# Performance work log

Measured on AMD Instinct MI355X. Metric: run time of the kernel, lower is better.

Reference implementation:

```python
import math
import jax, jax.numpy as jnp
import numpy as np

FACTOR = 5
N_HEADS = 8


def setup_inputs() -> dict:
    key = jax.random.key(0)
    ks = jax.random.split(key, 9)
    B, S, D = 4, 8192, 512
    s = 0.02
    x = jax.random.normal(ks[0], (B, S, D), jnp.float32)
    Wq = jax.random.normal(ks[1], (D, D), jnp.float32) * s
    bq = jax.random.normal(ks[2], (D,), jnp.float32) * s
    Wk = jax.random.normal(ks[3], (D, D), jnp.float32) * s
    bk = jax.random.normal(ks[4], (D,), jnp.float32) * s
    Wv = jax.random.normal(ks[5], (D, D), jnp.float32) * s
    bv = jax.random.normal(ks[6], (D,), jnp.float32) * s
    Wo = jax.random.normal(ks[7], (D, D), jnp.float32) * s
    bo = jax.random.normal(ks[8], (D,), jnp.float32) * s
    return {"x": x, "Wq": Wq, "bq": bq, "Wk": Wk, "bk": bk,
            "Wv": Wv, "bv": bv, "Wo": Wo, "bo": bo}


def reference(x, Wq, bq, Wk, bk, Wv, bv, Wo, bo):
    B, S, D = x.shape
    H = N_HEADS
    hd = D // H
    scale = hd ** -0.5

    def proj(W, b):
        # [B,S,D] -> [B,H,S,hd]
        return (x @ W + b).reshape(B, S, H, hd).transpose(0, 2, 1, 3)

    q = proj(Wq, bq)
    k = proj(Wk, bk)
    v = proj(Wv, bv)

    # number of "active" queries: O(log S)
    sampled = max(1, min(S, int(FACTOR * math.log(S + 1))))

    sparsity = jnp.sum(q * q, axis=-1)                    # [B,H,S]
    top_idx = jax.lax.top_k(sparsity, sampled)[1]         # [B,H,u]

    sel_q = jnp.take_along_axis(q, top_idx[..., None], axis=2)  # [B,H,u,hd]
    scores = jnp.einsum('bhud,bhsd->bhus', sel_q, k) * scale     # [B,H,u,S]
    attn = jax.nn.softmax(scores, axis=-1)
    sel_ctx = jnp.einsum('bhus,bhsd->bhud', attn, v)             # [B,H,u,hd]

    # default context = mean of values; overwrite rows of selected queries
    ctx = jnp.broadcast_to(v.mean(axis=2, keepdims=True), (B, H, S, hd))
    bi = jnp.arange(B)[:, None, None]
    hi = jnp.arange(H)[None, :, None]
    ctx = ctx.at[bi, hi, top_idx].set(sel_ctx)                   # scatter [B,H,S,hd]

    ctx = ctx.transpose(0, 2, 1, 3).reshape(B, S, D)
    return ctx @ Wo + bo
```

## Files before the change

### kernel.cpp

```cpp
#include <hip/hip_runtime.h>
#include <hip/hip_fp16.h>
#include <math.h>

#define B_ 4
#define S_ 8192
#define D_ 512
#define H_ 8
#define U_ 45
#define NCHUNK 16

typedef unsigned short ushortT;
typedef __attribute__((ext_vector_type(8))) _Float16 half8;
typedef __attribute__((ext_vector_type(4))) float f32x4;

__device__ __forceinline__ ushortT f2h(float f) {
    return __half_as_ushort(__float2half(f));
}
__device__ __forceinline__ float h2f(ushortT u) {
    return __half2float(__ushort_as_half(u));
}

__device__ __forceinline__ void gload_lds16(const ushortT* g, ushortT* l) {
    __builtin_amdgcn_global_load_lds(
        (const __attribute__((address_space(1))) void*)g,
        (__attribute__((address_space(3))) void*)l,
        16, 0, 0);
}

__global__ __launch_bounds__(256) void xconv(
    const float* __restrict__ X, ushortT* __restrict__ Xf,
    float* __restrict__ vsum, float* __restrict__ outbase)
{
    if (blockIdx.x == 0) {
        float4 z = {0.f, 0.f, 0.f, 0.f};
        *(float4*)&vsum[threadIdx.x * 8]        = z;
        *(float4*)&vsum[threadIdx.x * 8 + 4]    = z;
        *(float4*)&outbase[threadIdx.x * 8]     = z;
        *(float4*)&outbase[threadIdx.x * 8 + 4] = z;
    }
    size_t i = ((size_t)blockIdx.x * 256 + threadIdx.x) * 8;
    float4 a = *(const float4*)(X + i);
    float4 b = *(const float4*)(X + i + 4);
    *(ushort4*)(Xf + i)     = make_ushort4(f2h(a.x), f2h(a.y), f2h(a.z), f2h(a.w));
    *(ushort4*)(Xf + i + 4) = make_ushort4(f2h(b.x), f2h(b.y), f2h(b.z), f2h(b.w));
}

__global__ __launch_bounds__(256) void wprep(
    const float* __restrict__ Wq, const float* __restrict__ Wk,
    const float* __restrict__ Wv,
    ushortT* __restrict__ WqT, ushortT* __restrict__ WkT,
    ushortT* __restrict__ WvT)
{
    __shared__ float t[32][33];
    const int z = blockIdx.z;
    const float* W = (z == 0) ? Wq : (z == 1) ? Wk : Wv;
    ushortT* O = (z == 0) ? WqT : (z == 1) ? WkT : WvT;
    const int tx = threadIdx.x & 31, ty4 = (threadIdx.x >> 5) * 4;
    const int r0 = blockIdx.y * 32, c0 = blockIdx.x * 32;
#pragma unroll
    for (int i = 0; i < 4; ++i)
        t[ty4 + i][tx] = W[(size_t)(r0 + ty4 + i) * 512 + c0 + tx];
    __syncthreads();
#pragma unroll
    for (int i = 0; i < 4; ++i)
        O[(size_t)(c0 + ty4 + i) * 512 + r0 + tx] = f2h(t[tx][ty4 + i]);
}

__global__ __launch_bounds__(256, 2) void qkv_mfma(
    const ushortT* __restrict__ Xf,
    const ushortT* __restrict__ WqT, const ushortT* __restrict__ WkT,
    const ushortT* __restrict__ WvT,
    const float* __restrict__ bq, const float* __restrict__ bk,
    const float* __restrict__ bv,
    ushortT* __restrict__ Qbuf, ushortT* __restrict__ Kbuf,
    ushortT* __restrict__ VT,
    float* __restrict__ sparsity, float* __restrict__ vsum)
{
    __shared__ ushortT lds[2 * 128 * 64];
    ushortT* As = lds;
    ushortT* Bs = lds + 8192;

    const int tid  = threadIdx.x;
    const int w    = tid >> 6, lane = tid & 63;
    const int quad = lane >> 4, c16 = lane & 15;
    const int wr   = w >> 1,  wc  = w & 1;
    const int mat  = blockIdx.y >> 2;
    const int nt   = blockIdx.y & 3;
    const int m0   = blockIdx.x * 128;
    const int n0   = nt * 128;

    const int srowL = lane >> 3;
    const int slc   = (((lane & 7) - (srowL & 7)) & 7) * 8;
    const int rrot  = c16 & 7;

    const ushortT* Ag = (mat == 2) ? WvT : Xf;
    const ushortT* Bg = (mat == 0) ? WqT : (mat == 1) ? WkT : Xf;
    const int arow0 = (mat == 2) ? n0 : m0;
    const int brow0 = (mat == 2) ? m0 : n0;

    f32x4 acc[4][4];
#pragma unroll
    for (int i = 0; i < 4; ++i)
#pragma unroll
        for (int j = 0; j < 4; ++j) acc[i][j] = (f32x4){0.f, 0.f, 0.f, 0.f};

    for (int k0 = 0; k0 < 512; k0 += 64) {
        __syncthreads();
#pragma unroll
        for (int c = 0; c < 4; ++c) {
            const int R = c * 32 + w * 8 + srowL;
            const int lbase = c * 2048 + w * 512;
            gload_lds16(Ag + (size_t)(arow0 + R) * 512 + k0 + slc, As + lbase);
            gload_lds16(Bg + (size_t)(brow0 + R) * 512 + k0 + slc, Bs + lbase);
        }
        __syncthreads();
#pragma unroll
        for (int kk = 0; kk < 2; ++kk) {
            const int phk = (((kk * 4 + quad) + rrot) & 7) * 8;
            half8 af[4], bf[4];
#pragma unroll
            for (int i = 0; i < 4; ++i) {
                af[i] = *(const half8*)&As[(wr * 64 + i * 16 + c16) * 64 + phk];
                bf[i] = *(const half8*)&Bs[(wc * 64 + i * 16 + c16) * 64 + phk];
            }
#pragma unroll
            for (int i = 0; i < 4; ++i)
#pragma unroll
                for (int j = 0; j < 4; ++j)
                    acc[i][j] = __builtin_amdgcn_mfma_f32_16x16x32_f16(af[i], bf[j], acc[i][j], 0, 0, 0);
        }
    }

    if (mat == 0) {
        const int b = m0 >> 13;
        const int head = (n0 + wc * 64) >> 6;
        float bb[4];
#pragma unroll
        for (int j = 0; j < 4; ++j) bb[j] = bq[n0 + wc * 64 + j * 16 + c16];
        ushortT* qbase = Qbuf + ((size_t)(b * 8 + head) * 8192) * 64;
#pragma unroll
        for (int i = 0; i < 4; ++i)
#pragma unroll
            for (int r = 0; r < 4; ++r) {
                const int s = (m0 & 8191) + wr * 64 + i * 16 + quad * 4 + r;
                float p = 0.f;
#pragma unroll
                for (int j = 0; j < 4; ++j) {
                    float v = acc[i][j][r] + bb[j];
                    qbase[(size_t)s * 64 + j * 16 + c16] = f2h(v);
                    p = fmaf(v, v, p);
                }
                p += __shfl_xor(p, 1);
                p += __shfl_xor(p, 2);
                p += __shfl_xor(p, 4);
                p += __shfl_xor(p, 8);
                if (c16 == 0)
                    sparsity[((size_t)b * H_ + head) * S_ + s] = p;
            }
    } else if (mat == 1) {
        const int b = m0 >> 13;
        const int head = (n0 + wc * 64) >> 6;
        float bb[4];
#pragma unroll
        for (int j = 0; j < 4; ++j) bb[j] = bk[n0 + wc * 64 + j * 16 + c16];
        ushortT* kbase = Kbuf + ((size_t)(b * 8 + head) * 8192) * 64;
#pragma unroll
        for (int i = 0; i < 4; ++i)
#pragma unroll
            for (int r = 0; r < 4; ++r) {
                const int s = (m0 & 8191) + wr * 64 + i * 16 + quad * 4 + r;
#pragma unroll
                for (int j = 0; j < 4; ++j)
                    kbase[(size_t)s * 64 + j * 16 + c16] = f2h(acc[i][j][r] + bb[j]);
            }
    } else {
        const int b = m0 >> 13;
        const int sbase = (m0 & 8191) + wc * 64;
#pragma unroll
        for (int i = 0; i < 4; ++i)
#pragma unroll
            for (int r = 0; r < 4; ++r) {
                const int dcol = n0 + wr * 64 + i * 16 + quad * 4 + r;
                const int head = dcol >> 6, dd = dcol & 63;
                const float biasv = bv[dcol];
                ushortT* vrow = VT + ((size_t)(b * 8 + head) * 64 + dd) * 8192;
                float vsa = 0.f;
#pragma unroll
                for (int j = 0; j < 4; ++j) {
                    float v = acc[i][j][r] + biasv;
                    vrow[sbase + j * 16 + c16] = f2h(v);
                    vsa += v;
                }
                vsa += __shfl_xor(vsa, 1);
                vsa += __shfl_xor(vsa, 2);
                vsa += __shfl_xor(vsa, 4);
                vsa += __shfl_xor(vsa, 8);
                if (c16 == 0) atomicAdd(&vsum[b * 512 + dcol], vsa);
            }
    }
}

__global__ __launch_bounds__(256) void topk_kernel(
    const float* __restrict__ sparsity, int* __restrict__ topidx)
{
    __shared__ unsigned vals[S_];
    __shared__ unsigned hist[8][256];
    __shared__ int ssum[256];
    __shared__ unsigned prefix_s;
    __shared__ int need_s;
    __shared__ int cnt_gt_s, cnt_eq_s;
    __shared__ int eqidx[64];
    const int bh = blockIdx.x, tid = threadIdx.x;
    const unsigned* sp = (const unsigned*)(sparsity + (size_t)bh * S_);
    for (int i = tid; i < S_; i += 256) vals[i] = sp[i];

    unsigned prefix = 0;
    int need = U_;
    const int rep = tid & 7;
    for (int level = 0; level < 4; ++level) {
        const int shift = 24 - level * 8;
#pragma unroll
        for (int r = 0; r < 8; ++r) hist[r][tid] = 0;
        __syncthreads();
        const unsigned pmask = (level == 0) ? 0u : (0xFFFFFFFFu << (shift + 8));
        for (int i = tid; i < S_; i += 256) {
            unsigned v = vals[i];
            if ((v & pmask) == prefix)
                atomicAdd(&hist[rep][(v >> shift) & 255], 1u);
        }
        __syncthreads();
        int bs = 0;
#pragma unroll
        for (int r = 0; r < 8; ++r) bs += (int)hist[r][tid];
        ssum[tid] = bs;
        __syncthreads();
        for (int off = 1; off < 256; off <<= 1) {
            int add = (tid + off < 256) ? ssum[tid + off] : 0;
            __syncthreads();
            ssum[tid] += add;
            __syncthreads();
        }
        int snext = (tid == 255) ? 0 : ssum[tid + 1];
        if (ssum[tid] >= need && snext < need) {
            prefix_s = prefix | ((unsigned)tid << shift);
            need_s = need - snext;
        }
        __syncthreads();
        prefix = prefix_s;
        need = need_s;
        __syncthreads();
    }
    const unsigned T = prefix;
    if (tid == 0) { cnt_gt_s = 0; cnt_eq_s = 0; }
    __syncthreads();
    for (int i = tid; i < S_; i += 256) {
        unsigned v = vals[i];
        if (v > T) {
            int p = atomicAdd(&cnt_gt_s, 1);
            topidx[bh * U_ + p] = i;
        } else if (v == T) {
            int p = atomicAdd(&cnt_eq_s, 1);
            if (p < 64) eqidx[p] = i;
        }
    }
    __syncthreads();
    if (tid == 0) {
        int rem = U_ - cnt_gt_s;
        int n = cnt_eq_s < 64 ? cnt_eq_s : 64;
        for (int a = 0; a < rem; ++a) {
            int best = 1 << 30, bj = 0;
            for (int j = 0; j < n; ++j)
                if (eqidx[j] < best) { best = eqidx[j]; bj = j; }
            topidx[bh * U_ + cnt_gt_s + a] = best;
            eqidx[bj] = 1 << 30;
        }
    }
}

__global__ __launch_bounds__(256, 2) void attn_mfma(
    const ushortT* __restrict__ Qbuf, const ushortT* __restrict__ Kbuf,
    const ushortT* __restrict__ VT, const int* __restrict__ topidx,
    float* __restrict__ pl, float* __restrict__ pacc)
{
    __shared__ float sc[48 * 132];
    __shared__ ushortT Qb[48 * 72];

    const int tid = threadIdx.x;
    const int w = tid >> 6, lane = tid & 63;
    const int quad = lane >> 4, c16 = lane & 15;
    const int bh = blockIdx.y;
    const int s_base = blockIdx.x * 512;

    for (int i = tid; i < 48 * 64; i += 256) {
        int q = i >> 6, d = i & 63;
        float v = 0.f;
        if (q < U_) {
            int s = topidx[bh * U_ + q];
            v = h2f(Qbuf[((size_t)bh * 8192 + s) * 64 + d]) * 0.125f;
        }
        Qb[q * 72 + d] = f2h(v);
    }

    f32x4 O[3];
#pragma unroll
    for (int mt = 0; mt < 3; ++mt) O[mt] = (f32x4){0.f, 0.f, 0.f, 0.f};
    float lacc[12];
#pragma unroll
    for (int qi = 0; qi < 12; ++qi) lacc[qi] = 0.f;

    __syncthreads();

    half8 qa[3][2];
#pragma unroll
    for (int mt = 0; mt < 3; ++mt)
#pragma unroll
        for (int kk = 0; kk < 2; ++kk)
            qa[mt][kk] = *(const half8*)&Qb[(mt * 16 + c16) * 72 + kk * 32 + quad * 8];

    const ushortT* kb  = Kbuf + (size_t)bh * 8192 * 64;
    const ushortT* vtb = VT + ((size_t)bh * 64 + w * 16 + c16) * 8192;

    for (int ci = 0; ci < 4; ++ci) {
        const int s0 = s_base + ci * 128;

        half8 kf[2][2];
#pragma unroll
        for (int nt2 = 0; nt2 < 2; ++nt2)
#pragma unroll
            for (int kk = 0; kk < 2; ++kk)
                kf[nt2][kk] = *(const half8*)&kb[
                    (size_t)(s0 + w * 32 + nt2 * 16 + c16) * 64 + kk * 32 + quad * 8];
        f32x4 sacc[3][2];
#pragma unroll
        for (int mt = 0; mt < 3; ++mt)
#pragma unroll
            for (int nt2 = 0; nt2 < 2; ++nt2) {
                sacc[mt][nt2] = (f32x4){0.f, 0.f, 0.f, 0.f};
#pragma unroll
                for (int kk = 0; kk < 2; ++kk)
                    sacc[mt][nt2] = __builtin_amdgcn_mfma_f32_16x16x32_f16(
                        qa[mt][kk], kf[nt2][kk], sacc[mt][nt2], 0, 0, 0);
            }
#pragma unroll
        for (int mt = 0; mt < 3; ++mt)
#pragma unroll
            for (int nt2 = 0; nt2 < 2; ++nt2)
#pragma unroll
                for (int r = 0; r < 4; ++r)
                    sc[(mt * 16 + quad * 4 + r) * 132 + w * 32 + nt2 * 16 + c16] =
                        sacc[mt][nt2][r];
        __syncthreads();

        half8 vb[4];
#pragma unroll
        for (int kk = 0; kk < 4; ++kk)
            vb[kk] = *(const half8*)&vtb[s0 + kk * 32 + quad * 8];

#pragma unroll
        for (int qi = 0; qi < 12; ++qi) {
            const int q = w * 12 + qi;
            float x0 = sc[q * 132 + lane];
            float x1 = sc[q * 132 + 64 + lane];
            ushortT u0 = f2h(__expf(x0));
            ushortT u1 = f2h(__expf(x1));
            lacc[qi] += h2f(u0) + h2f(u1);
            ushortT* pr = (ushortT*)&sc[q * 132];
            pr[lane] = u0;
            pr[lane + 64] = u1;
        }
        __syncthreads();

#pragma unroll
        for (int mt = 0; mt < 3; ++mt)
#pragma unroll
            for (int kk = 0; kk < 4; ++kk) {
                half8 pa = *(const half8*)((const ushortT*)sc +
                    (size_t)(mt * 16 + c16) * 264 + kk * 32 + quad * 8);
                O[mt] = __builtin_amdgcn_mfma_f32_16x16x32_f16(pa, vb[kk], O[mt], 0, 0, 0);
            }
        __syncthreads();
    }

#pragma unroll
    for (int mt = 0; mt < 3; ++mt)
#pragma unroll
        for (int r = 0; r < 4; ++r) {
            const int q = mt * 16 + quad * 4 + r;
            if (q < U_)
                pacc[(((size_t)bh * NCHUNK + blockIdx.x) * U_ + q) * 64 + w * 16 + c16] =
                    O[mt][r];
        }
#pragma unroll
    for (int qi = 0; qi < 12; ++qi) {
        const int q = w * 12 + qi;
        float ssum = lacc[qi];
#pragma unroll
        for (int off = 1; off < 64; off <<= 1) ssum += __shfl_xor(ssum, off);
        if (lane == 0 && q < U_)
            pl[((size_t)bh * NCHUNK + blockIdx.x) * U_ + q] = ssum;
    }
}

__global__ __launch_bounds__(512) void outbase_kernel(
    const float* __restrict__ vsum, const float* __restrict__ Wo,
    const float* __restrict__ bo, float* __restrict__ outbase)
{
    const int b = blockIdx.x, ks = blockIdx.y, d = threadIdx.x;
    float acc = (ks == 0) ? bo[d] : 0.f;
    const int r0 = ks * 128;
    for (int r = r0; r < r0 + 128; ++r) {
        float mv = vsum[b * 512 + r] * (1.0f / S_);
        acc = fmaf(mv, Wo[(size_t)r * 512 + d], acc);
    }
    atomicAdd(&outbase[b * 512 + d], acc);
}

__global__ __launch_bounds__(256) void fill_kernel(
    const float* __restrict__ outbase, float* __restrict__ out)
{
    size_t gid = (size_t)blockIdx.x * 256 + threadIdx.x;
    size_t e0 = gid * 4;
    int b = (int)(e0 >> 22);
    int col = (int)(e0 & 511);
    float4 v = *(const float4*)&outbase[b * 512 + col];
    *(float4*)&out[e0] = v;
}

__global__ __launch_bounds__(512) void corr_out_kernel(
    const float* __restrict__ pl, const float* __restrict__ pacc,
    const float* __restrict__ vsum, const float* __restrict__ Wo,
    const int* __restrict__ topidx, float* __restrict__ out)
{
    __shared__ float corrS[64];
    const int q = blockIdx.x, bh = blockIdx.y;
    const int b = bh >> 3, h = bh & 7, tid = threadIdx.x;
    if (tid < 64) {
        float L = 0.f, a = 0.f;
        for (int c = 0; c < NCHUNK; ++c) {
            L += pl[((size_t)bh * NCHUNK + c) * U_ + q];
            a += pacc[(((size_t)bh * NCHUNK + c) * U_ + q) * 64 + tid];
        }
        corrS[tid] = a / L - vsum[b * 512 + h * 64 + tid] * (1.0f / S_);
    }
    __syncthreads();
    const int s = topidx[bh * U_ + q];
    const int d = tid;
    float delta = 0.f;
#pragma unroll
    for (int r = 0; r < 64; ++r)
        delta = fmaf(corrS[r], Wo[(size_t)(h * 64 + r) * 512 + d], delta);
    atomicAdd(&out[((size_t)b * S_ + s) * 512 + d], delta);
}

extern "C" void kernel_launch(void* const* d_in, const int* in_sizes, int n_in,
                              void* d_out, int out_size, void* d_ws, size_t ws_size,
                              hipStream_t stream)
{
    const float* X  = (const float*)d_in[0];
    const float* Wq = (const float*)d_in[1];
    const float* bq = (const float*)d_in[2];
    const float* Wk = (const float*)d_in[3];
    const float* bk = (const float*)d_in[4];
    const float* Wv = (const float*)d_in[5];
    const float* bv = (const float*)d_in[6];
    const float* Wo = (const float*)d_in[7];
    const float* bo = (const float*)d_in[8];
    float* out = (float*)d_out;

    char* ws = (char*)d_ws;
    size_t off = 0;
    auto alloc = [&](size_t bytes) {
        void* p = ws + off;
        off = (off + bytes + 255) & ~(size_t)255;
        return p;
    };
    ushortT* Xf   = (ushortT*)alloc((size_t)B_ * S_ * D_ * 2);
    ushortT* Qbuf = (ushortT*)alloc((size_t)B_ * S_ * D_ * 2);
    ushortT* Kbuf = (ushortT*)alloc((size_t)B_ * S_ * D_ * 2);
    ushortT* VT   = (ushortT*)alloc((size_t)B_ * S_ * D_ * 2);
    ushortT* WqT  = (ushortT*)alloc((size_t)D_ * D_ * 2);
    ushortT* WkT  = (ushortT*)alloc((size_t)D_ * D_ * 2);
    ushortT* WvT  = (ushortT*)alloc((size_t)D_ * D_ * 2);
    float* sparsity = (float*)alloc((size_t)B_ * H_ * S_ * 4);
    int*   topidx   = (int*)alloc((size_t)B_ * H_ * U_ * 4);
    float* pl       = (float*)alloc((size_t)B_ * H_ * NCHUNK * U_ * 4);
    float* pacc     = (float*)alloc((size_t)B_ * H_ * NCHUNK * U_ * 64 * 4);
    float* vsum     = (float*)alloc((size_t)B_ * 512 * 4);
    float* outbase  = (float*)alloc((size_t)B_ * 512 * 4);

    xconv<<<(B_ * S_ * D_) / (256 * 8), 256, 0, stream>>>(X, Xf, vsum, outbase);
    wprep<<<dim3(16, 16, 3), 256, 0, stream>>>(Wq, Wk, Wv, WqT, WkT, WvT);
    qkv_mfma<<<dim3(256, 12), 256, 0, stream>>>(Xf, WqT, WkT, WvT,
                                                bq, bk, bv, Qbuf, Kbuf, VT,
                                                sparsity, vsum);
    topk_kernel<<<B_ * H_, 256, 0, stream>>>(sparsity, topidx);
    attn_mfma<<<dim3(NCHUNK, B_ * H_), 256, 0, stream>>>(Qbuf, Kbuf, VT, topidx,
                                                         pl, pacc);
    outbase_kernel<<<dim3(B_, 4), 512, 0, stream>>>(vsum, Wo, bo, outbase);
    fill_kernel<<<(B_ * S_ * D_ / 4 + 255) / 256, 256, 0, stream>>>(outbase, out);
    corr_out_kernel<<<dim3(U_, B_ * H_), 512, 0, stream>>>(pl, pacc, vsum, Wo,
                                                           topidx, out);
}
```

Before: 290.7 us.

## Fuse QKV projections into one GEMM pass and merge small prep kernels

The three Q/K/V projection GEMMs now run inside a single block per output tile, so each X tile is loaded into LDS once and reused against all three weight tiles. The grid shrinks from 12 to 4 column tiles. V is now transposed through LDS so global stores are coalesced 16-byte writes instead of scattered 2-byte ones. The X conversion and weight transpose are merged into one launch, and the outbase GEMV rides on extra blocks of the top-k kernel, which removes launches. The cost is 48 accumulator vectors per thread and 64KB of LDS, which lowers occupancy, and only 1024 blocks for the GEMM.

Result: no change. 292.8 us (+0.7%).

```diff
diff --git a/kernel.cpp b/kernel.cpp
--- a/kernel.cpp
+++ b/kernel.cpp
@@ -11,6 +11,7 @@
 
 typedef unsigned short ushortT;
 typedef __attribute__((ext_vector_type(8))) _Float16 half8;
+typedef __attribute__((ext_vector_type(8))) unsigned short ushort8;
 typedef __attribute__((ext_vector_type(4))) float f32x4;
 
 __device__ __forceinline__ ushortT f2h(float f) {
@@ -27,43 +28,44 @@
         16, 0, 0);
 }
 
-__global__ __launch_bounds__(256) void xconv(
+__global__ __launch_bounds__(256) void prep_kernel(
     const float* __restrict__ X, ushortT* __restrict__ Xf,
-    float* __restrict__ vsum, float* __restrict__ outbase)
-{
-    if (blockIdx.x == 0) {
-        float4 z = {0.f, 0.f, 0.f, 0.f};
-        *(float4*)&vsum[threadIdx.x * 8]        = z;
-        *(float4*)&vsum[threadIdx.x * 8 + 4]    = z;
-        *(float4*)&outbase[threadIdx.x * 8]     = z;
-        *(float4*)&outbase[threadIdx.x * 8 + 4] = z;
-    }
-    size_t i = ((size_t)blockIdx.x * 256 + threadIdx.x) * 8;
-    float4 a = *(const float4*)(X + i);
-    float4 b = *(const float4*)(X + i + 4);
-    *(ushort4*)(Xf + i)     = make_ushort4(f2h(a.x), f2h(a.y), f2h(a.z), f2h(a.w));
-    *(ushort4*)(Xf + i + 4) = make_ushort4(f2h(b.x), f2h(b.y), f2h(b.z), f2h(b.w));
-}
-
-__global__ __launch_bounds__(256) void wprep(
     const float* __restrict__ Wq, const float* __restrict__ Wk,
     const float* __restrict__ Wv,
     ushortT* __restrict__ WqT, ushortT* __restrict__ WkT,
-    ushortT* __restrict__ WvT)
+    ushortT* __restrict__ WvT,
+    float* __restrict__ vsum, float* __restrict__ outbase)
 {
     __shared__ float t[32][33];
-    const int z = blockIdx.z;
-    const float* W = (z == 0) ? Wq : (z == 1) ? Wk : Wv;
-    ushortT* O = (z == 0) ? WqT : (z == 1) ? WkT : WvT;
-    const int tx = threadIdx.x & 31, ty4 = (threadIdx.x >> 5) * 4;
-    const int r0 = blockIdx.y * 32, c0 = blockIdx.x * 32;
-#pragma unroll
-    for (int i = 0; i < 4; ++i)
-        t[ty4 + i][tx] = W[(size_t)(r0 + ty4 + i) * 512 + c0 + tx];
-    __syncthreads();
-#pragma unroll
-    for (int i = 0; i < 4; ++i)
-        O[(size_t)(c0 + ty4 + i) * 512 + r0 + tx] = f2h(t[tx][ty4 + i]);
+    const int bx = blockIdx.x;
+    if (bx < 8192) {
+        if (bx == 0) {
+            float4 z = {0.f, 0.f, 0.f, 0.f};
+            *(float4*)&vsum[threadIdx.x * 8]        = z;
+            *(float4*)&vsum[threadIdx.x * 8 + 4]    = z;
+            *(float4*)&outbase[threadIdx.x * 8]     = z;
+            *(float4*)&outbase[threadIdx.x * 8 + 4] = z;
+        }
+        size_t i = ((size_t)bx * 256 + threadIdx.x) * 8;
+        float4 a = *(const float4*)(X + i);
+        float4 b = *(const float4*)(X + i + 4);
+        *(ushort4*)(Xf + i)     = make_ushort4(f2h(a.x), f2h(a.y), f2h(a.z), f2h(a.w));
+        *(ushort4*)(Xf + i + 4) = make_ushort4(f2h(b.x), f2h(b.y), f2h(b.z), f2h(b.w));
+    } else {
+        const int idx = bx - 8192;
+        const int z = idx >> 8, rem = idx & 255;
+        const int r0 = (rem >> 4) * 32, c0 = (rem & 15) * 32;
+        const float* W = (z == 0) ? Wq : (z == 1) ? Wk : Wv;
+        ushortT* O = (z == 0) ? WqT : (z == 1) ? WkT : WvT;
+        const int tx = threadIdx.x & 31, ty4 = (threadIdx.x >> 5) * 4;
+#pragma unroll
+        for (int i = 0; i < 4; ++i)
+            t[ty4 + i][tx] = W[(size_t)(r0 + ty4 + i) * 512 + c0 + tx];
+        __syncthreads();
+#pragma unroll
+        for (int i = 0; i < 4; ++i)
+            O[(size_t)(c0 + ty4 + i) * 512 + r0 + tx] = f2h(t[tx][ty4 + i]);
+    }
 }
 
 __global__ __launch_bounds__(256, 2) void qkv_mfma(
@@ -76,33 +78,33 @@
     ushortT* __restrict__ VT,
     float* __restrict__ sparsity, float* __restrict__ vsum)
 {
-    __shared__ ushortT lds[2 * 128 * 64];
+    __shared__ ushortT lds[4 * 128 * 64];
     ushortT* As = lds;
-    ushortT* Bs = lds + 8192;
+    ushortT* Bq = lds + 8192;
+    ushortT* Bk = lds + 16384;
+    ushortT* Bv = lds + 24576;
 
     const int tid  = threadIdx.x;
     const int w    = tid >> 6, lane = tid & 63;
     const int quad = lane >> 4, c16 = lane & 15;
     const int wr   = w >> 1,  wc  = w & 1;
-    const int mat  = blockIdx.y >> 2;
-    const int nt   = blockIdx.y & 3;
     const int m0   = blockIdx.x * 128;
-    const int n0   = nt * 128;
+    const int n0   = blockIdx.y * 128;
+    const int b    = m0 >> 13;
 
     const int srowL = lane >> 3;
     const int slc   = (((lane & 7) - (srowL & 7)) & 7) * 8;
     const int rrot  = c16 & 7;
 
-    const ushortT* Ag = (mat == 2) ? WvT : Xf;
-    const ushortT* Bg = (mat == 0) ? WqT : (mat == 1) ? WkT : Xf;
-    const int arow0 = (mat == 2) ? n0 : m0;
-    const int brow0 = (mat == 2) ? m0 : n0;
-
-    f32x4 acc[4][4];
+    f32x4 accQ[4][4], accK[4][4], accV[4][4];
 #pragma unroll
     for (int i = 0; i < 4; ++i)
 #pragma unroll
-        for (int j = 0; j < 4; ++j) acc[i][j] = (f32x4){0.f, 0.f, 0.f, 0.f};
+        for (int j = 0; j < 4; ++j) {
+            accQ[i][j] = (f32x4){0.f, 0.f, 0.f, 0.f};
+            accK[i][j] = (f32x4){0.f, 0.f, 0.f, 0.f};
+            accV[i][j] = (f32x4){0.f, 0.f, 0.f, 0.f};
+        }
 
     for (int k0 = 0; k0 < 512; k0 += 64) {
         __syncthreads();
@@ -110,29 +112,56 @@
         for (int c = 0; c < 4; ++c) {
             const int R = c * 32 + w * 8 + srowL;
             const int lbase = c * 2048 + w * 512;
-            gload_lds16(Ag + (size_t)(arow0 + R) * 512 + k0 + slc, As + lbase);
-            gload_lds16(Bg + (size_t)(brow0 + R) * 512 + k0 + slc, Bs + lbase);
+            gload_lds16(Xf  + (size_t)(m0 + R) * 512 + k0 + slc, As + lbase);
+            gload_lds16(WqT + (size_t)(n0 + R) * 512 + k0 + slc, Bq + lbase);
+            gload_lds16(WkT + (size_t)(n0 + R) * 512 + k0 + slc, Bk + lbase);
+            gload_lds16(WvT + (size_t)(n0 + R) * 512 + k0 + slc, Bv + lbase);
         }
         __syncthreads();
 #pragma unroll
         for (int kk = 0; kk < 2; ++kk) {
             const int phk = (((kk * 4 + quad) + rrot) & 7) * 8;
-            half8 af[4], bf[4];
-#pragma unroll
-            for (int i = 0; i < 4; ++i) {
+            half8 af[4];
+#pragma unroll
+            for (int i = 0; i < 4; ++i)
                 af[i] = *(const half8*)&As[(wr * 64 + i * 16 + c16) * 64 + phk];
-                bf[i] = *(const half8*)&Bs[(wc * 64 + i * 16 + c16) * 64 + phk];
-            }
-#pragma unroll
-            for (int i = 0; i < 4; ++i)
-#pragma unroll
-                for (int j = 0; j < 4; ++j)
-                    acc[i][j] = __builtin_amdgcn_mfma_f32_16x16x32_f16(af[i], bf[j], acc[i][j], 0, 0, 0);
-        }
-    }
-
-    if (mat == 0) {
-        const int b = m0 >> 13;
+            {
+                half8 bf[4];
+#pragma unroll
+                for (int i = 0; i < 4; ++i)
+                    bf[i] = *(const half8*)&Bq[(wc * 64 + i * 16 + c16) * 64 + phk];
+#pragma unroll
+                for (int i = 0; i < 4; ++i)
+#pragma unroll
+                    for (int j = 0; j < 4; ++j)
+                        accQ[i][j] = __builtin_amdgcn_mfma_f32_16x16x32_f16(af[i], bf[j], accQ[i][j], 0, 0, 0);
+            }
+            {
+                half8 bf[4];
+#pragma unroll
+                for (int i = 0; i < 4; ++i)
+                    bf[i] = *(const half8*)&Bk[(wc * 64 + i * 16 + c16) * 64 + phk];
+#pragma unroll
+                for (int i = 0; i < 4; ++i)
+#pragma unroll
+                    for (int j = 0; j < 4; ++j)
+                        accK[i][j] = __builtin_amdgcn_mfma_f32_16x16x32_f16(af[i], bf[j], accK[i][j], 0, 0, 0);
+            }
+            {
+                half8 bf[4];
+#pragma unroll
+                for (int i = 0; i < 4; ++i)
+                    bf[i] = *(const half8*)&Bv[(wc * 64 + i * 16 + c16) * 64 + phk];
+#pragma unroll
+                for (int i = 0; i < 4; ++i)
+#pragma unroll
+                    for (int j = 0; j < 4; ++j)
+                        accV[i][j] = __builtin_amdgcn_mfma_f32_16x16x32_f16(af[i], bf[j], accV[i][j], 0, 0, 0);
+            }
+        }
+    }
+
+    {
         const int head = (n0 + wc * 64) >> 6;
         float bb[4];
 #pragma unroll
@@ -146,7 +175,7 @@
                 float p = 0.f;
 #pragma unroll
                 for (int j = 0; j < 4; ++j) {
-                    float v = acc[i][j][r] + bb[j];
+                    float v = accQ[i][j][r] + bb[j];
                     qbase[(size_t)s * 64 + j * 16 + c16] = f2h(v);
                     p = fmaf(v, v, p);
                 }
@@ -157,8 +186,8 @@
                 if (c16 == 0)
                     sparsity[((size_t)b * H_ + head) * S_ + s] = p;
             }
-    } else if (mat == 1) {
-        const int b = m0 >> 13;
+    }
+    {
         const int head = (n0 + wc * 64) >> 6;
         float bb[4];
 #pragma unroll
@@ -171,37 +200,45 @@
                 const int s = (m0 & 8191) + wr * 64 + i * 16 + quad * 4 + r;
 #pragma unroll
                 for (int j = 0; j < 4; ++j)
-                    kbase[(size_t)s * 64 + j * 16 + c16] = f2h(acc[i][j][r] + bb[j]);
-            }
-    } else {
-        const int b = m0 >> 13;
-        const int sbase = (m0 & 8191) + wc * 64;
-#pragma unroll
-        for (int i = 0; i < 4; ++i)
-#pragma unroll
-            for (int r = 0; r < 4; ++r) {
-                const int dcol = n0 + wr * 64 + i * 16 + quad * 4 + r;
-                const int head = dcol >> 6, dd = dcol & 63;
-                const float biasv = bv[dcol];
-                ushortT* vrow = VT + ((size_t)(b * 8 + head) * 64 + dd) * 8192;
-                float vsa = 0.f;
-#pragma unroll
-                for (int j = 0; j < 4; ++j) {
-                    float v = acc[i][j][r] + biasv;
-                    vrow[sbase + j * 16 + c16] = f2h(v);
+                    kbase[(size_t)s * 64 + j * 16 + c16] = f2h(accK[i][j][r] + bb[j]);
+            }
+    }
+    {
+        __syncthreads();
+        ushortT* Vt = lds;
+#pragma unroll
+        for (int j = 0; j < 4; ++j) {
+            const int dcol = wc * 64 + j * 16 + c16;
+            const float biasv = bv[n0 + dcol];
+            float vsa = 0.f;
+#pragma unroll
+            for (int i = 0; i < 4; ++i)
+#pragma unroll
+                for (int r = 0; r < 4; ++r) {
+                    const int s = wr * 64 + i * 16 + quad * 4 + r;
+                    float v = accV[i][j][r] + biasv;
+                    Vt[dcol * 136 + s] = f2h(v);
                     vsa += v;
                 }
-                vsa += __shfl_xor(vsa, 1);
-                vsa += __shfl_xor(vsa, 2);
-                vsa += __shfl_xor(vsa, 4);
-                vsa += __shfl_xor(vsa, 8);
-                if (c16 == 0) atomicAdd(&vsum[b * 512 + dcol], vsa);
-            }
+            vsa += __shfl_xor(vsa, 16);
+            vsa += __shfl_xor(vsa, 32);
+            if (quad == 0) atomicAdd(&vsum[b * 512 + n0 + dcol], vsa);
+        }
+        __syncthreads();
+        const int dcol = tid & 127, part = tid >> 7;
+        const int g = n0 + dcol, head = g >> 6, dd = g & 63;
+        ushortT* vrow = VT + ((size_t)(b * 8 + head) * 64 + dd) * 8192
+                        + (m0 & 8191) + part * 64;
+#pragma unroll
+        for (int u = 0; u < 8; ++u)
+            *(ushort8*)&vrow[u * 8] = *(const ushort8*)&Vt[dcol * 136 + part * 64 + u * 8];
     }
 }
 
 __global__ __launch_bounds__(256) void topk_kernel(
-    const float* __restrict__ sparsity, int* __restrict__ topidx)
+    const float* __restrict__ sparsity, int* __restrict__ topidx,
+    const float* __restrict__ vsum, const float* __restrict__ Wo,
+    const float* __restrict__ bo, float* __restrict__ outbase)
 {
     __shared__ unsigned vals[S_];
     __shared__ unsigned hist[8][256];
@@ -210,7 +247,23 @@
     __shared__ int need_s;
     __shared__ int cnt_gt_s, cnt_eq_s;
     __shared__ int eqidx[64];
-    const int bh = blockIdx.x, tid = threadIdx.x;
+    const int tid = threadIdx.x;
+
+    if (blockIdx.x >= 32) {
+        const int idx = blockIdx.x - 32;
+        const int b = idx >> 3, ks = (idx & 7) >> 1, dh = idx & 1;
+        const int d = dh * 256 + tid;
+        float acc = (ks == 0) ? bo[d] : 0.f;
+        const int r0 = ks * 128;
+        for (int r = r0; r < r0 + 128; ++r) {
+            float mv = vsum[b * 512 + r] * (1.0f / S_);
+            acc = fmaf(mv, Wo[(size_t)r * 512 + d], acc);
+        }
+        atomicAdd(&outbase[b * 512 + d], acc);
+        return;
+    }
+
+    const int bh = blockIdx.x;
     const unsigned* sp = (const unsigned*)(sparsity + (size_t)bh * S_);
     for (int i = tid; i < S_; i += 256) vals[i] = sp[i];
 
@@ -399,20 +452,6 @@
         if (lane == 0 && q < U_)
             pl[((size_t)bh * NCHUNK + blockIdx.x) * U_ + q] = ssum;
     }
-}
-
-__global__ __launch_bounds__(512) void outbase_kernel(
-    const float* __restrict__ vsum, const float* __restrict__ Wo,
-    const float* __restrict__ bo, float* __restrict__ outbase)
-{
-    const int b = blockIdx.x, ks = blockIdx.y, d = threadIdx.x;
-    float acc = (ks == 0) ? bo[d] : 0.f;
-    const int r0 = ks * 128;
-    for (int r = r0; r < r0 + 128; ++r) {
-        float mv = vsum[b * 512 + r] * (1.0f / S_);
-        acc = fmaf(mv, Wo[(size_t)r * 512 + d], acc);
-    }
-    atomicAdd(&outbase[b * 512 + d], acc);
 }
 
 __global__ __launch_bounds__(256) void fill_kernel(
@@ -488,15 +527,14 @@
     float* vsum     = (float*)alloc((size_t)B_ * 512 * 4);
     float* outbase  = (float*)alloc((size_t)B_ * 512 * 4);
 
-    xconv<<<(B_ * S_ * D_) / (256 * 8), 256, 0, stream>>>(X, Xf, vsum, outbase);
-    wprep<<<dim3(16, 16, 3), 256, 0, stream>>>(Wq, Wk, Wv, WqT, WkT, WvT);
-    qkv_mfma<<<dim3(256, 12), 256, 0, stream>>>(Xf, WqT, WkT, WvT,
-                                                bq, bk, bv, Qbuf, Kbuf, VT,
-                                                sparsity, vsum);
-    topk_kernel<<<B_ * H_, 256, 0, stream>>>(sparsity, topidx);
+    prep_kernel<<<8960, 256, 0, stream>>>(X, Xf, Wq, Wk, Wv, WqT, WkT, WvT,
+                                          vsum, outbase);
+    qkv_mfma<<<dim3(256, 4), 256, 0, stream>>>(Xf, WqT, WkT, WvT,
+                                               bq, bk, bv, Qbuf, Kbuf, VT,
+                                               sparsity, vsum);
+    topk_kernel<<<64, 256, 0, stream>>>(sparsity, topidx, vsum, Wo, bo, outbase);
     attn_mfma<<<dim3(NCHUNK, B_ * H_), 256, 0, stream>>>(Qbuf, Kbuf, VT, topidx,
                                                          pl, pacc);
-    outbase_kernel<<<dim3(B_, 4), 512, 0, stream>>>(vsum, Wo, bo, outbase);
     fill_kernel<<<(B_ * S_ * D_ / 4 + 255) / 256, 256, 0, stream>>>(outbase, out);
     corr_out_kernel<<<dim3(U_, B_ * H_), 512, 0, stream>>>(pl, pacc, vsum, Wo,
                                                            topidx, out);
```
